# Kernel optimization log

Hardware: AMD Instinct MI355X
Metric: run time of the kernel (lower is better)

The kernel has to match this reference:

```python
import jax, jax.numpy as jnp
import numpy as np
import math

N = 524288          # number of 3D query points
L = 4               # grid_level = num_sin_layers - 2
F = 8               # feat_dim per hash level
T = 1 << 19         # log2_hashmap_size = 19 (hardcoded in module)
H = 64              # SIREN hidden width (dims entries)
OUT_DIM = 128       # sin_dims[-1] * size_factor
BOUND = 1.0
BASE_RES = 16.0
PER_LEVEL_SCALE = 2.0
BASE_SIGMA = 5.0
EXP_SIGMA = 2.0
SIN_W0 = 30.0
SIN_W1 = 30.0

_PRIMES = jnp.array([1, 2654435761, 805459861], dtype=jnp.uint32)  # tcnn hash primes
_CORNERS = np.array([[(i >> 2) & 1, (i >> 1) & 1, i & 1] for i in range(8)])
_CORNERS_U = jnp.asarray(_CORNERS, dtype=jnp.uint32)
_CORNERS_F = jnp.asarray(_CORNERS, dtype=jnp.float32)


def hash_grid(pos01, table):
    """Multi-resolution hash-grid encoding. pos01: [N,3] in [0,1], table: [L,T,F] -> [L,N,F]."""
    res = jnp.floor(BASE_RES * PER_LEVEL_SCALE ** jnp.arange(L, dtype=jnp.float32))  # [L]

    def level(tab, r):
        p = pos01 * r                       # [N,3]
        p0 = jnp.floor(p)
        f = p - p0                          # trilinear fractions
        c = p0.astype(jnp.uint32)[:, None, :] + _CORNERS_U[None]   # [N,8,3] corner coords
        hp = c * _PRIMES
        h = (hp[..., 0] ^ hp[..., 1] ^ hp[..., 2]) & jnp.uint32(T - 1)  # [N,8] hash indices
        feats = tab[h]                      # [N,8,F]
        w = jnp.prod(jnp.where(_CORNERS_F[None] > 0, f[:, None, :], 1.0 - f[:, None, :]), axis=-1)  # [N,8]
        return jnp.einsum('nc,ncf->nf', w, feats)

    return jax.vmap(level)(table, res)


def setup_inputs() -> dict:
    key = jax.random.key(0)
    ks = jax.random.split(key, 10)
    in_pos = jax.random.uniform(ks[0], (N, 3), minval=-BOUND, maxval=BOUND)
    table = jax.random.uniform(ks[1], (L, T, F), minval=-1e-4, maxval=1e-4)
    # ffn[i] = randn(F, H) * base_sigma * exp_sigma**i
    scales = BASE_SIGMA * EXP_SIGMA ** jnp.arange(L, dtype=jnp.float32)
    ffn = jax.random.normal(ks[2], (L, F, H)) * scales[:, None, None]
    # SIREN init: first layer U(-1/fan_in, 1/fan_in); others U(-sqrt(6/fan_in)/w0, ...)
    W0 = jax.random.uniform(ks[3], (3, H), minval=-1.0 / 3.0, maxval=1.0 / 3.0)
    b0 = jax.random.uniform(ks[4], (H,), minval=-1.0 / math.sqrt(3.0), maxval=1.0 / math.sqrt(3.0))
    bw = math.sqrt(6.0 / H) / SIN_W0
    Ws = jax.random.uniform(ks[5], (L, H, H), minval=-bw, maxval=bw)
    bs = jax.random.uniform(ks[6], (L, H), minval=-1.0 / math.sqrt(H), maxval=1.0 / math.sqrt(H))
    bo = math.sqrt(6.0 / H) / SIN_W1
    Wout = jax.random.uniform(ks[7], (L, H, OUT_DIM), minval=-bo, maxval=bo)
    bout = jax.random.uniform(ks[8], (L, OUT_DIM), minval=-1.0 / math.sqrt(H), maxval=1.0 / math.sqrt(H))
    return {"in_pos": in_pos, "table": table, "ffn": ffn, "W0": W0, "b0": b0,
            "Ws": Ws, "bs": bs, "Wout": Wout, "bout": bout}


def reference(in_pos, table, ffn, W0, b0, Ws, bs, Wout, bout):
    x = in_pos / BOUND                              # SIREN input in [-1,1]
    pos01 = (in_pos + BOUND) / (2.0 * BOUND)        # grid input in [0,1]
    grid_x = hash_grid(pos01, table)                # [L,N,F]
    # Fourier feature branch: sin(2*pi * grid_x @ ffn)
    emb = jnp.sin(2.0 * math.pi * jnp.einsum('lnf,lfh->lnh', grid_x, ffn))  # [L,N,H]
    # first SIREN layer (layer 0)
    x = jnp.sin(SIN_W0 * (x @ W0 + b0))             # [N,H]
    x_out = jnp.zeros((x.shape[0], OUT_DIM), x.dtype)
    for l in range(L):                              # layers 1..num_sin_layers-2
        x = jnp.sin(SIN_W0 * (x @ Ws[l] + bs[l]))
        x = emb[l] + x                              # residual add of grid Fourier features
        x_out = x_out + jnp.sin(SIN_W1 * (x @ Wout[l] + bout[l]))  # accumulate output head
    return x_out
```

## Files before the change

### kernel.cpp

```cpp
#include <hip/hip_runtime.h>
#include <cstdint>
#include <cstddef>

#define NLVL 4
#define TSIZE (1u << 19)
#define NH 64
#define NOUT 128
#define MBLK 128
#define PANEL 12800
#define SFOLD 4.774648292756860f

typedef _Float16 f16x8 __attribute__((ext_vector_type(8)));
typedef _Float16 f16x2 __attribute__((ext_vector_type(2)));
typedef float f32x4 __attribute__((ext_vector_type(4)));
typedef unsigned short u16x8 __attribute__((ext_vector_type(8)));
typedef unsigned int u32x4 __attribute__((ext_vector_type(4)));

__device__ __forceinline__ float fsin01(float x) {
    return __builtin_amdgcn_sinf(__builtin_amdgcn_fractf(x));
}
__device__ __forceinline__ unsigned short h2u(_Float16 h) {
    return __builtin_bit_cast(unsigned short, h);
}
__device__ __forceinline__ unsigned int pk16(float a, float b) {
    return __builtin_bit_cast(unsigned int, __builtin_amdgcn_cvt_pkrtz(a, b));
}
__device__ __forceinline__ void gl_lds16(const _Float16* g, _Float16* l) {
    __builtin_amdgcn_global_load_lds(
        (const __attribute__((address_space(1))) void*)g,
        (__attribute__((address_space(3))) void*)l, 16, 0, 0);
}

__global__ void prep_weights(const float* __restrict__ Ws,
                             const float* __restrict__ Wout,
                             const float* __restrict__ ffn,
                             _Float16* __restrict__ ws)
{
    int i = blockIdx.x * 256 + threadIdx.x;
    if (i < 16384) {
        int l = i >> 12, r = i & 4095, k = r >> 6, c = r & 63;
        ws[l * PANEL + ((c * 64 + k) ^ ((c & 7) << 3))] = (_Float16)(Ws[i] * SFOLD);
    } else if (i < 18432) {
        int j = i - 16384;
        int l = j >> 9, r = j & 511, k = r >> 6, c = r & 63;
        ws[l * PANEL + 4096 + c * 8 + k] = (_Float16)(ffn[j] * 0.000244140625f);
    } else if (i < 51200) {
        int j = i - 18432;
        int l = j >> 13, rem = j & 8191, k = rem >> 7, c = rem & 127;
        int ct = c >> 4, r15 = c & 15, kb = k >> 5, hi4 = (k >> 3) & 3, jj = k & 7;
        ws[l * PANEL + 4608 + (ct * 2 + kb) * 512 + hi4 * 128 + r15 * 8 + jj] =
            (_Float16)(Wout[j] * SFOLD);
    }
}

__global__ __launch_bounds__(256) void prep_table(const float* __restrict__ table,
                                                  _Float16* __restrict__ tab16)
{
    int i = blockIdx.x * 256 + threadIdx.x;
    float v = __builtin_nontemporal_load(table + i);
    tab16[i] = (_Float16)(v * 4096.f);
}

template <bool F16TAB>
__global__ __launch_bounds__(512, 2)
void ffb_main(const float* __restrict__ in_pos,
              const float* __restrict__ table,
              const _Float16* __restrict__ tab16,
              const float* __restrict__ W0,
              const float* __restrict__ b0,
              const float* __restrict__ bs,
              const float* __restrict__ bout,
              const _Float16* __restrict__ wsg,
              float* __restrict__ out)
{
    __shared__ __align__(16) _Float16 wbuf[2][PANEL];
    __shared__ __align__(16) unsigned short gS[NLVL][MBLK][8];

    const int tid = threadIdx.x;
    const int pbase = blockIdx.x * MBLK;
    const int lane = tid & 63;
    const int wv = tid >> 6;
    const int r15 = lane & 15;
    const int hi4 = lane >> 4;

    {
        const int p = tid & (MBLK - 1);
        const int lv = tid >> 7;
        const float px = in_pos[3 * (pbase + p) + 0];
        const float py = in_pos[3 * (pbase + p) + 1];
        const float pz = in_pos[3 * (pbase + p) + 2];
        const float qx = (px + 1.f) * 0.5f, qy = (py + 1.f) * 0.5f, qz = (pz + 1.f) * 0.5f;
        const uint32_t P1 = 2654435761u, P2 = 805459861u;

        const float res = (float)(16 << lv);
        float gx = qx * res, gy = qy * res, gz = qz * res;
        float fx0 = floorf(gx), fy0 = floorf(gy), fz0 = floorf(gz);
        float fx = gx - fx0, fy = gy - fy0, fz = gz - fz0;
        uint32_t ux = (uint32_t)fx0, uy = (uint32_t)fy0, uz = (uint32_t)fz0;
        uint32_t hx0 = ux, hx1 = ux + 1u;
        uint32_t hy0 = uy * P1, hy1 = hy0 + P1;
        uint32_t hz0 = uz * P2, hz1 = hz0 + P2;

        uint32_t hh[8];
        float    wgt[8];
        #pragma unroll
        for (int c = 0; c < 8; ++c) {
            hh[c] = (((c & 4) ? hx1 : hx0) ^ ((c & 2) ? hy1 : hy0)
                     ^ ((c & 1) ? hz1 : hz0)) & (TSIZE - 1u);
            wgt[c] = ((c & 4) ? fx : 1.f - fx) * ((c & 2) ? fy : 1.f - fy)
                   * ((c & 1) ? fz : 1.f - fz);
        }

        if (F16TAB) {
            const _Float16* tl = tab16 + (size_t)lv * TSIZE * 8;
            u16x8 vv[8];
            #pragma unroll
            for (int c = 0; c < 8; ++c)
                vv[c] = *(const u16x8*)(tl + (size_t)hh[c] * 8);
            f16x2 acc2[4];
            #pragma unroll
            for (int q = 0; q < 4; ++q) acc2[q] = (f16x2){(_Float16)0.f, (_Float16)0.f};
            #pragma unroll
            for (int c = 0; c < 8; ++c) {
                _Float16 wh = (_Float16)wgt[c];
                f16x2 ww = {wh, wh};
                const f16x2* vp = (const f16x2*)&vv[c];
                #pragma unroll
                for (int q = 0; q < 4; ++q) acc2[q] = acc2[q] + ww * vp[q];
            }
            *(u16x8*)&gS[lv][p][0] = *(u16x8*)&acc2[0];
        } else {
            const float* tl = table + (size_t)lv * TSIZE * 8;
            float g[8];
            #pragma unroll
            for (int q = 0; q < 8; ++q) g[q] = 0.f;
            #pragma unroll
            for (int c = 0; c < 8; ++c) {
                const float4* fp = (const float4*)(tl + (size_t)hh[c] * 8);
                float4 va = fp[0], vb = fp[1];
                float w = wgt[c];
                g[0] = fmaf(w, va.x, g[0]); g[1] = fmaf(w, va.y, g[1]);
                g[2] = fmaf(w, va.z, g[2]); g[3] = fmaf(w, va.w, g[3]);
                g[4] = fmaf(w, vb.x, g[4]); g[5] = fmaf(w, vb.y, g[5]);
                g[6] = fmaf(w, vb.z, g[6]); g[7] = fmaf(w, vb.w, g[7]);
            }
            u16x8 gv;
            #pragma unroll
            for (int q = 0; q < 8; ++q)
                gv[q] = h2u((_Float16)(g[q] * 4096.f));
            *(u16x8*)&gS[lv][p][0] = gv;
        }
    }

    auto stage = [&](int l) {
        const _Float16* src = wsg + l * PANEL;
        _Float16* dst = &wbuf[l & 1][0];
        #pragma unroll
        for (int i = 0; i < 3; ++i)
            gl_lds16(src + (i * 512 + tid) * 8, dst + (i * 512 + (tid & ~63)) * 8);
        if (tid < 64)
            gl_lds16(src + (1536 + tid) * 8, dst + 1536 * 8);
    };
    stage(0);

    f16x8 Xb[2];
    {
        const int pp = pbase + wv * 16 + r15;
        const float lpx = in_pos[3 * pp + 0];
        const float lpy = in_pos[3 * pp + 1];
        const float lpz = in_pos[3 * pp + 2];
        #pragma unroll
        for (int kb = 0; kb < 2; ++kb) {
            f16x8 v;
            #pragma unroll
            for (int j = 0; j < 8; ++j) {
                const int f = kb * 32 + hi4 * 8 + j;
                float a = b0[f] + lpx * W0[f] + lpy * W0[64 + f] + lpz * W0[128 + f];
                v[j] = (_Float16)fsin01(a * SFOLD);
            }
            Xb[kb] = v;
        }
    }
    __syncthreads();

    const int idxA = ((lane & 16) << 3) + r15 * 4;
    const int idxB = idxA + 64;
    const bool hiHalf = (lane & 32) != 0;

    f16x2 accP[8][2];
    #pragma unroll
    for (int ct = 0; ct < 8; ++ct)
        #pragma unroll
        for (int s = 0; s < 2; ++s) accP[ct][s] = (f16x2){(_Float16)0.f, (_Float16)0.f};

    #pragma unroll 1
    for (int lvl = 0; lvl < NLVL; ++lvl) {
        if (lvl < NLVL - 1) stage(lvl + 1);
        const _Float16* wp = &wbuf[lvl & 1][0];

        f16x8 gB;
        {
            f16x8 z;
            #pragma unroll
            for (int q = 0; q < 8; ++q) z[q] = (_Float16)0.f;
            if (lane < 16)
                z = *(const f16x8*)&gS[lvl][wv * 16 + lane][0];
            gB = z;
        }

        unsigned int P[4][2];
        #pragma unroll
        for (int ct = 0; ct < 4; ++ct) {
            const int i0 = ((ct * 16 + r15) * 64 + hi4 * 8) ^ ((r15 & 7) << 3);
            f16x8 A0 = *(const f16x8*)&wp[i0];
            f16x8 A1 = *(const f16x8*)&wp[i0 ^ 32];
            f16x8 Af;
            #pragma unroll
            for (int q = 0; q < 8; ++q) Af[q] = (_Float16)0.f;
            if (lane < 16)
                Af = *(const f16x8*)&wp[4096 + (ct * 16 + lane) * 8];
            float4 bs4 = *(const float4*)&bs[lvl * 64 + ct * 16 + hi4 * 4];

            f32x4 c1 = {bs4.x * SFOLD, bs4.y * SFOLD, bs4.z * SFOLD, bs4.w * SFOLD};
            c1 = __builtin_amdgcn_mfma_f32_16x16x32_f16(A0, Xb[0], c1, 0, 0, 0);
            c1 = __builtin_amdgcn_mfma_f32_16x16x32_f16(A1, Xb[1], c1, 0, 0, 0);
            f32x4 c2 = {0.f, 0.f, 0.f, 0.f};
            c2 = __builtin_amdgcn_mfma_f32_16x16x32_f16(Af, gB, c2, 0, 0, 0);

            P[ct][0] = pk16(fsin01(c1[0]) + fsin01(c2[0]),
                            fsin01(c1[1]) + fsin01(c2[1]));
            P[ct][1] = pk16(fsin01(c1[2]) + fsin01(c2[2]),
                            fsin01(c1[3]) + fsin01(c2[3]));
        }

        #pragma unroll
        for (int kb = 0; kb < 2; ++kb) {
            unsigned int w[4];
            #pragma unroll
            for (int m = 0; m < 4; ++m) {
                int idx = (m < 2) ? idxA : idxB;
                int lo = __builtin_amdgcn_ds_bpermute(idx, (int)P[2 * kb + 0][m & 1]);
                int hi = __builtin_amdgcn_ds_bpermute(idx, (int)P[2 * kb + 1][m & 1]);
                w[m] = (unsigned int)(hiHalf ? hi : lo);
            }
            Xb[kb] = __builtin_bit_cast(f16x8, (u32x4){w[0], w[1], w[2], w[3]});
        }

        #pragma unroll
        for (int ct = 0; ct < 8; ++ct) {
            const _Float16* bp = &wp[4608 + (ct * 2) * 512 + hi4 * 128 + r15 * 8];
            f16x8 B0 = *(const f16x8*)bp;
            f16x8 B1 = *(const f16x8*)(bp + 512);
            float bov = bout[lvl * 128 + ct * 16 + r15] * SFOLD;
            f32x4 c = {bov, bov, bov, bov};
            c = __builtin_amdgcn_mfma_f32_16x16x32_f16(Xb[0], B0, c, 0, 0, 0);
            c = __builtin_amdgcn_mfma_f32_16x16x32_f16(Xb[1], B1, c, 0, 0, 0);
            accP[ct][0] = accP[ct][0] +
                __builtin_bit_cast(f16x2, pk16(fsin01(c[0]), fsin01(c[1])));
            accP[ct][1] = accP[ct][1] +
                __builtin_bit_cast(f16x2, pk16(fsin01(c[2]), fsin01(c[3])));
        }

        if (lvl < NLVL - 1) __syncthreads();
    }

    #pragma unroll
    for (int s = 0; s < 2; ++s)
        #pragma unroll
        for (int r2 = 0; r2 < 2; ++r2) {
            int row = pbase + wv * 16 + hi4 * 4 + s * 2 + r2;
            #pragma unroll
            for (int ct = 0; ct < 8; ++ct) {
                float v = (float)accP[ct][s][r2];
                __builtin_nontemporal_store(v, &out[(size_t)row * 128 + ct * 16 + r15]);
            }
        }
}

extern "C" void kernel_launch(void* const* d_in, const int* in_sizes, int n_in,
                              void* d_out, int out_size, void* d_ws, size_t ws_size,
                              hipStream_t stream) {
    const float* in_pos = (const float*)d_in[0];
    const float* table  = (const float*)d_in[1];
    const float* ffn    = (const float*)d_in[2];
    const float* W0     = (const float*)d_in[3];
    const float* b0     = (const float*)d_in[4];
    const float* Ws     = (const float*)d_in[5];
    const float* bs     = (const float*)d_in[6];
    const float* Wout   = (const float*)d_in[7];
    const float* bout   = (const float*)d_in[8];
    float* out = (float*)d_out;
    _Float16* ws = (_Float16*)d_ws;

    const size_t need = 65536u * 2u + (size_t)NLVL * TSIZE * 8u * 2u;
    const bool f16tab = (ws_size >= need);
    _Float16* tab16 = ws + 65536;

    prep_weights<<<dim3(200), dim3(256), 0, stream>>>(Ws, Wout, ffn, ws);

    const int n = in_sizes[0] / 3;
    if (f16tab) {
        prep_table<<<dim3((NLVL * TSIZE * 8) / 256), dim3(256), 0, stream>>>(table, tab16);
        ffb_main<true><<<dim3(n / MBLK), dim3(512), 0, stream>>>(
            in_pos, table, tab16, W0, b0, bs, bout, ws, out);
    } else {
        ffb_main<false><<<dim3(n / MBLK), dim3(512), 0, stream>>>(
            in_pos, table, tab16, W0, b0, bs, bout, ws, out);
    }
}
```

Before: 256.4 us.

## Split hash-grid gather into a separate kernel and prefetch per-level features

Moves the hash-grid corner gather and trilinear blend into a standalone high-occupancy kernel that writes per-level f16 features to workspace. The main MLP kernel then reads these features from global memory, prefetching the next level's values one iteration ahead, and no longer needs the LDS staging buffer for them. The aim is to stop the random table gathers from stalling the MFMA-heavy main kernel. In exchange it adds a kernel launch and a round trip of the intermediate features through global memory, and this path is only taken when the workspace is large enough.

```diff
diff --git a/kernel.cpp b/kernel.cpp
--- a/kernel.cpp
+++ b/kernel.cpp
@@ -4,6 +4,8 @@
 
 #define NLVL 4
 #define TSIZE (1u << 19)
+#define NPTS (1 << 19)
+#define PLOG 19
 #define NH 64
 #define NOUT 128
 #define MBLK 128
@@ -61,11 +63,60 @@
     tab16[i] = (_Float16)(v * 4096.f);
 }
 
-template <bool F16TAB>
+__global__ __launch_bounds__(256, 4)
+void gather_g(const float* __restrict__ in_pos,
+              const _Float16* __restrict__ tab16,
+              _Float16* __restrict__ gSg)
+{
+    const int gid = blockIdx.x * 256 + threadIdx.x;
+    const int point = gid & (NPTS - 1);
+    const int lv = gid >> PLOG;
+
+    const float px = in_pos[3 * point + 0];
+    const float py = in_pos[3 * point + 1];
+    const float pz = in_pos[3 * point + 2];
+    const float qx = (px + 1.f) * 0.5f, qy = (py + 1.f) * 0.5f, qz = (pz + 1.f) * 0.5f;
+    const uint32_t P1 = 2654435761u, P2 = 805459861u;
+
+    const float res = (float)(16 << lv);
+    float gx = qx * res, gy = qy * res, gz = qz * res;
+    float fx0 = floorf(gx), fy0 = floorf(gy), fz0 = floorf(gz);
+    float fx = gx - fx0, fy = gy - fy0, fz = gz - fz0;
+    uint32_t ux = (uint32_t)fx0, uy = (uint32_t)fy0, uz = (uint32_t)fz0;
+    uint32_t hx0 = ux, hx1 = ux + 1u;
+    uint32_t hy0 = uy * P1, hy1 = hy0 + P1;
+    uint32_t hz0 = uz * P2, hz1 = hz0 + P2;
+
+    const _Float16* tl = tab16 + (size_t)lv * TSIZE * 8;
+    u16x8 vv[8];
+    #pragma unroll
+    for (int c = 0; c < 8; ++c) {
+        uint32_t h = (((c & 4) ? hx1 : hx0) ^ ((c & 2) ? hy1 : hy0)
+                      ^ ((c & 1) ? hz1 : hz0)) & (TSIZE - 1u);
+        vv[c] = *(const u16x8*)(tl + (size_t)h * 8);
+    }
+    f16x2 acc2[4];
+    #pragma unroll
+    for (int q = 0; q < 4; ++q) acc2[q] = (f16x2){(_Float16)0.f, (_Float16)0.f};
+    #pragma unroll
+    for (int c = 0; c < 8; ++c) {
+        float w = ((c & 4) ? fx : 1.f - fx) * ((c & 2) ? fy : 1.f - fy)
+                * ((c & 1) ? fz : 1.f - fz);
+        _Float16 wh = (_Float16)w;
+        f16x2 ww = {wh, wh};
+        const f16x2* vp = (const f16x2*)&vv[c];
+        #pragma unroll
+        for (int q = 0; q < 4; ++q) acc2[q] = acc2[q] + ww * vp[q];
+    }
+    *(u16x8*)&gSg[(size_t)gid * 8] = *(u16x8*)&acc2[0];
+}
+
+template <int MODE>
 __global__ __launch_bounds__(512, 2)
 void ffb_main(const float* __restrict__ in_pos,
               const float* __restrict__ table,
               const _Float16* __restrict__ tab16,
+              const _Float16* __restrict__ gSg,
               const float* __restrict__ W0,
               const float* __restrict__ b0,
               const float* __restrict__ bs,
@@ -74,7 +125,7 @@
               float* __restrict__ out)
 {
     __shared__ __align__(16) _Float16 wbuf[2][PANEL];
-    __shared__ __align__(16) unsigned short gS[NLVL][MBLK][8];
+    __shared__ __align__(16) unsigned short gS[MODE < 2 ? NLVL * MBLK * 8 : 4];
 
     const int tid = threadIdx.x;
     const int pbase = blockIdx.x * MBLK;
@@ -83,7 +134,7 @@
     const int r15 = lane & 15;
     const int hi4 = lane >> 4;
 
-    {
+    if (MODE < 2) {
         const int p = tid & (MBLK - 1);
         const int lv = tid >> 7;
         const float px = in_pos[3 * (pbase + p) + 0];
@@ -111,7 +162,7 @@
                    * ((c & 1) ? fz : 1.f - fz);
         }
 
-        if (F16TAB) {
+        if (MODE == 1) {
             const _Float16* tl = tab16 + (size_t)lv * TSIZE * 8;
             u16x8 vv[8];
             #pragma unroll
@@ -128,7 +179,7 @@
                 #pragma unroll
                 for (int q = 0; q < 4; ++q) acc2[q] = acc2[q] + ww * vp[q];
             }
-            *(u16x8*)&gS[lv][p][0] = *(u16x8*)&acc2[0];
+            *(u16x8*)&gS[(lv * MBLK + p) * 8] = *(u16x8*)&acc2[0];
         } else {
             const float* tl = table + (size_t)lv * TSIZE * 8;
             float g[8];
@@ -148,7 +199,7 @@
             #pragma unroll
             for (int q = 0; q < 8; ++q)
                 gv[q] = h2u((_Float16)(g[q] * 4096.f));
-            *(u16x8*)&gS[lv][p][0] = gv;
+            *(u16x8*)&gS[(lv * MBLK + p) * 8] = gv;
         }
     }
 
@@ -183,6 +234,19 @@
     }
     __syncthreads();
 
+    auto loadg = [&](int l) -> f16x8 {
+        f16x8 z;
+        #pragma unroll
+        for (int q = 0; q < 8; ++q) z[q] = (_Float16)0.f;
+        if (lane < 16) {
+            if (MODE == 2)
+                z = *(const f16x8*)&gSg[((size_t)l * NPTS + pbase + wv * 16 + lane) * 8];
+            else
+                z = *(const f16x8*)&gS[(l * MBLK + wv * 16 + lane) * 8];
+        }
+        return z;
+    };
+
     const int idxA = ((lane & 16) << 3) + r15 * 4;
     const int idxB = idxA + 64;
     const bool hiHalf = (lane & 32) != 0;
@@ -193,20 +257,13 @@
         #pragma unroll
         for (int s = 0; s < 2; ++s) accP[ct][s] = (f16x2){(_Float16)0.f, (_Float16)0.f};
 
+    f16x8 gBcur = loadg(0);
+
     #pragma unroll 1
     for (int lvl = 0; lvl < NLVL; ++lvl) {
         if (lvl < NLVL - 1) stage(lvl + 1);
+        f16x8 gBnext = (lvl < NLVL - 1) ? loadg(lvl + 1) : gBcur;
         const _Float16* wp = &wbuf[lvl & 1][0];
-
-        f16x8 gB;
-        {
-            f16x8 z;
-            #pragma unroll
-            for (int q = 0; q < 8; ++q) z[q] = (_Float16)0.f;
-            if (lane < 16)
-                z = *(const f16x8*)&gS[lvl][wv * 16 + lane][0];
-            gB = z;
-        }
 
         unsigned int P[4][2];
         #pragma unroll
@@ -225,7 +282,7 @@
             c1 = __builtin_amdgcn_mfma_f32_16x16x32_f16(A0, Xb[0], c1, 0, 0, 0);
             c1 = __builtin_amdgcn_mfma_f32_16x16x32_f16(A1, Xb[1], c1, 0, 0, 0);
             f32x4 c2 = {0.f, 0.f, 0.f, 0.f};
-            c2 = __builtin_amdgcn_mfma_f32_16x16x32_f16(Af, gB, c2, 0, 0, 0);
+            c2 = __builtin_amdgcn_mfma_f32_16x16x32_f16(Af, gBcur, c2, 0, 0, 0);
 
             P[ct][0] = pk16(fsin01(c1[0]) + fsin01(c2[0]),
                             fsin01(c1[1]) + fsin01(c2[1]));
@@ -261,6 +318,7 @@
                 __builtin_bit_cast(f16x2, pk16(fsin01(c[2]), fsin01(c[3])));
         }
 
+        gBcur = gBnext;
         if (lvl < NLVL - 1) __syncthreads();
     }
 
@@ -292,19 +350,27 @@
     float* out = (float*)d_out;
     _Float16* ws = (_Float16*)d_ws;
 
-    const size_t need = 65536u * 2u + (size_t)NLVL * TSIZE * 8u * 2u;
-    const bool f16tab = (ws_size >= need);
+    const int n = in_sizes[0] / 3;
+    const size_t tabElems = (size_t)NLVL * TSIZE * 8;
+    const size_t gOff = 65536u + tabElems;
+    const size_t need1 = (65536u + tabElems) * 2u;
+    const size_t need2 = (gOff + (size_t)NLVL * n * 8) * 2u;
     _Float16* tab16 = ws + 65536;
+    _Float16* gSg   = ws + gOff;
 
     prep_weights<<<dim3(200), dim3(256), 0, stream>>>(Ws, Wout, ffn, ws);
 
-    const int n = in_sizes[0] / 3;
-    if (f16tab) {
-        prep_table<<<dim3((NLVL * TSIZE * 8) / 256), dim3(256), 0, stream>>>(table, tab16);
-        ffb_main<true><<<dim3(n / MBLK), dim3(512), 0, stream>>>(
-            in_pos, table, tab16, W0, b0, bs, bout, ws, out);
+    if (ws_size >= need2) {
+        prep_table<<<dim3(tabElems / 256), dim3(256), 0, stream>>>(table, tab16);
+        gather_g<<<dim3((NLVL * n) / 256), dim3(256), 0, stream>>>(in_pos, tab16, gSg);
+        ffb_main<2><<<dim3(n / MBLK), dim3(512), 0, stream>>>(
+            in_pos, table, tab16, gSg, W0, b0, bs, bout, ws, out);
+    } else if (ws_size >= need1) {
+        prep_table<<<dim3(tabElems / 256), dim3(256), 0, stream>>>(table, tab16);
+        ffb_main<1><<<dim3(n / MBLK), dim3(512), 0, stream>>>(
+            in_pos, table, tab16, gSg, W0, b0, bs, bout, ws, out);
     } else {
-        ffb_main<false><<<dim3(n / MBLK), dim3(512), 0, stream>>>(
-            in_pos, table, tab16, W0, b0, bs, bout, ws, out);
-    }
-}
+        ffb_main<0><<<dim3(n / MBLK), dim3(512), 0, stream>>>(
+            in_pos, table, tab16, gSg, W0, b0, bs, bout, ws, out);
+    }
+}
```

Result: no change. 258.2 us (+0.7%).

## Process four point tiles per block and prefetch next tile's hash gathers

Applied to the files above, without the earlier changes.

Each block now handles four consecutive 128-point tiles in a persistent loop, with double-buffered grid-feature LDS slots. The hash-table gathers for the next tile are issued before the current tile's MLP so their latency overlaps MFMA work. Weight panels keep cycling through the same double buffer across tiles. The cost is more live registers for the in-flight gathers, a quarter as many blocks, and extra LDS for the second gS slot, which may reduce occupancy and leave the GPU underfilled.

```diff
diff --git a/kernel.cpp b/kernel.cpp
--- a/kernel.cpp
+++ b/kernel.cpp
@@ -7,6 +7,7 @@
 #define NH 64
 #define NOUT 128
 #define MBLK 128
+#define TILES 4
 #define PANEL 12800
 #define SFOLD 4.774648292756860f
 
@@ -74,83 +75,97 @@
               float* __restrict__ out)
 {
     __shared__ __align__(16) _Float16 wbuf[2][PANEL];
-    __shared__ __align__(16) unsigned short gS[NLVL][MBLK][8];
+    __shared__ __align__(16) unsigned short gS[2][NLVL][MBLK][8];
 
     const int tid = threadIdx.x;
-    const int pbase = blockIdx.x * MBLK;
+    const int blkbase = blockIdx.x * (MBLK * TILES);
     const int lane = tid & 63;
     const int wv = tid >> 6;
     const int r15 = lane & 15;
     const int hi4 = lane >> 4;
 
-    {
-        const int p = tid & (MBLK - 1);
-        const int lv = tid >> 7;
-        const float px = in_pos[3 * (pbase + p) + 0];
-        const float py = in_pos[3 * (pbase + p) + 1];
-        const float pz = in_pos[3 * (pbase + p) + 2];
-        const float qx = (px + 1.f) * 0.5f, qy = (py + 1.f) * 0.5f, qz = (pz + 1.f) * 0.5f;
-        const uint32_t P1 = 2654435761u, P2 = 805459861u;
-
-        const float res = (float)(16 << lv);
-        float gx = qx * res, gy = qy * res, gz = qz * res;
+    const int p_g = tid & (MBLK - 1);
+    const int lv_g = tid >> 7;
+    const uint32_t P1 = 2654435761u, P2 = 805459861u;
+
+    u16x8 vv[8];
+    float gfx, gfy, gfz;
+
+    auto issueGather = [&](int pb) {
+        const float px = in_pos[3 * (pb + p_g) + 0];
+        const float py = in_pos[3 * (pb + p_g) + 1];
+        const float pz = in_pos[3 * (pb + p_g) + 2];
+        const float res = (float)(16 << lv_g);
+        float gx = (px + 1.f) * 0.5f * res;
+        float gy = (py + 1.f) * 0.5f * res;
+        float gz = (pz + 1.f) * 0.5f * res;
+        float fx0 = floorf(gx), fy0 = floorf(gy), fz0 = floorf(gz);
+        gfx = gx - fx0; gfy = gy - fy0; gfz = gz - fz0;
+        uint32_t ux = (uint32_t)fx0, uy = (uint32_t)fy0, uz = (uint32_t)fz0;
+        uint32_t hx0 = ux, hx1 = ux + 1u;
+        uint32_t hy0 = uy * P1, hy1 = hy0 + P1;
+        uint32_t hz0 = uz * P2, hz1 = hz0 + P2;
+        const _Float16* tl = tab16 + (size_t)lv_g * TSIZE * 8;
+        #pragma unroll
+        for (int c = 0; c < 8; ++c) {
+            uint32_t h = (((c & 4) ? hx1 : hx0) ^ ((c & 2) ? hy1 : hy0)
+                          ^ ((c & 1) ? hz1 : hz0)) & (TSIZE - 1u);
+            vv[c] = *(const u16x8*)(tl + (size_t)h * 8);
+        }
+    };
+    auto interpStore = [&](int slot) {
+        f16x2 acc2[4];
+        #pragma unroll
+        for (int q = 0; q < 4; ++q) acc2[q] = (f16x2){(_Float16)0.f, (_Float16)0.f};
+        #pragma unroll
+        for (int c = 0; c < 8; ++c) {
+            float w = ((c & 4) ? gfx : 1.f - gfx) * ((c & 2) ? gfy : 1.f - gfy)
+                    * ((c & 1) ? gfz : 1.f - gfz);
+            _Float16 wh = (_Float16)w;
+            f16x2 ww = {wh, wh};
+            const f16x2* vp = (const f16x2*)&vv[c];
+            #pragma unroll
+            for (int q = 0; q < 4; ++q) acc2[q] = acc2[q] + ww * vp[q];
+        }
+        *(u16x8*)&gS[slot][lv_g][p_g][0] = *(u16x8*)&acc2[0];
+    };
+    auto gatherF32 = [&](int pb, int slot) {
+        const float px = in_pos[3 * (pb + p_g) + 0];
+        const float py = in_pos[3 * (pb + p_g) + 1];
+        const float pz = in_pos[3 * (pb + p_g) + 2];
+        const float res = (float)(16 << lv_g);
+        float gx = (px + 1.f) * 0.5f * res;
+        float gy = (py + 1.f) * 0.5f * res;
+        float gz = (pz + 1.f) * 0.5f * res;
         float fx0 = floorf(gx), fy0 = floorf(gy), fz0 = floorf(gz);
         float fx = gx - fx0, fy = gy - fy0, fz = gz - fz0;
         uint32_t ux = (uint32_t)fx0, uy = (uint32_t)fy0, uz = (uint32_t)fz0;
         uint32_t hx0 = ux, hx1 = ux + 1u;
         uint32_t hy0 = uy * P1, hy1 = hy0 + P1;
         uint32_t hz0 = uz * P2, hz1 = hz0 + P2;
-
-        uint32_t hh[8];
-        float    wgt[8];
+        const float* tl = table + (size_t)lv_g * TSIZE * 8;
+        float g[8];
+        #pragma unroll
+        for (int q = 0; q < 8; ++q) g[q] = 0.f;
         #pragma unroll
         for (int c = 0; c < 8; ++c) {
-            hh[c] = (((c & 4) ? hx1 : hx0) ^ ((c & 2) ? hy1 : hy0)
-                     ^ ((c & 1) ? hz1 : hz0)) & (TSIZE - 1u);
-            wgt[c] = ((c & 4) ? fx : 1.f - fx) * ((c & 2) ? fy : 1.f - fy)
-                   * ((c & 1) ? fz : 1.f - fz);
-        }
-
-        if (F16TAB) {
-            const _Float16* tl = tab16 + (size_t)lv * TSIZE * 8;
-            u16x8 vv[8];
-            #pragma unroll
-            for (int c = 0; c < 8; ++c)
-                vv[c] = *(const u16x8*)(tl + (size_t)hh[c] * 8);
-            f16x2 acc2[4];
-            #pragma unroll
-            for (int q = 0; q < 4; ++q) acc2[q] = (f16x2){(_Float16)0.f, (_Float16)0.f};
-            #pragma unroll
-            for (int c = 0; c < 8; ++c) {
-                _Float16 wh = (_Float16)wgt[c];
-                f16x2 ww = {wh, wh};
-                const f16x2* vp = (const f16x2*)&vv[c];
-                #pragma unroll
-                for (int q = 0; q < 4; ++q) acc2[q] = acc2[q] + ww * vp[q];
-            }
-            *(u16x8*)&gS[lv][p][0] = *(u16x8*)&acc2[0];
-        } else {
-            const float* tl = table + (size_t)lv * TSIZE * 8;
-            float g[8];
-            #pragma unroll
-            for (int q = 0; q < 8; ++q) g[q] = 0.f;
-            #pragma unroll
-            for (int c = 0; c < 8; ++c) {
-                const float4* fp = (const float4*)(tl + (size_t)hh[c] * 8);
-                float4 va = fp[0], vb = fp[1];
-                float w = wgt[c];
-                g[0] = fmaf(w, va.x, g[0]); g[1] = fmaf(w, va.y, g[1]);
-                g[2] = fmaf(w, va.z, g[2]); g[3] = fmaf(w, va.w, g[3]);
-                g[4] = fmaf(w, vb.x, g[4]); g[5] = fmaf(w, vb.y, g[5]);
-                g[6] = fmaf(w, vb.z, g[6]); g[7] = fmaf(w, vb.w, g[7]);
-            }
-            u16x8 gv;
-            #pragma unroll
-            for (int q = 0; q < 8; ++q)
-                gv[q] = h2u((_Float16)(g[q] * 4096.f));
-            *(u16x8*)&gS[lv][p][0] = gv;
-        }
-    }
+            uint32_t h = (((c & 4) ? hx1 : hx0) ^ ((c & 2) ? hy1 : hy0)
+                          ^ ((c & 1) ? hz1 : hz0)) & (TSIZE - 1u);
+            float w = ((c & 4) ? fx : 1.f - fx) * ((c & 2) ? fy : 1.f - fy)
+                    * ((c & 1) ? fz : 1.f - fz);
+            const float4* fp = (const float4*)(tl + (size_t)h * 8);
+            float4 va = fp[0], vb = fp[1];
+            g[0] = fmaf(w, va.x, g[0]); g[1] = fmaf(w, va.y, g[1]);
+            g[2] = fmaf(w, va.z, g[2]); g[3] = fmaf(w, va.w, g[3]);
+            g[4] = fmaf(w, vb.x, g[4]); g[5] = fmaf(w, vb.y, g[5]);
+            g[6] = fmaf(w, vb.z, g[6]); g[7] = fmaf(w, vb.w, g[7]);
+        }
+        u16x8 gv;
+        #pragma unroll
+        for (int q = 0; q < 8; ++q)
+            gv[q] = h2u((_Float16)(g[q] * 4096.f));
+        *(u16x8*)&gS[slot][lv_g][p_g][0] = gv;
+    };
 
     auto stage = [&](int l) {
         const _Float16* src = wsg + l * PANEL;
@@ -161,11 +176,10 @@
         if (tid < 64)
             gl_lds16(src + (1536 + tid) * 8, dst + 1536 * 8);
     };
-    stage(0);
 
     f16x8 Xb[2];
-    {
-        const int pp = pbase + wv * 16 + r15;
+    auto layer0 = [&](int pb) {
+        const int pp = pb + wv * 16 + r15;
         const float lpx = in_pos[3 * pp + 0];
         const float lpy = in_pos[3 * pp + 1];
         const float lpz = in_pos[3 * pp + 2];
@@ -180,101 +194,121 @@
             }
             Xb[kb] = v;
         }
-    }
+    };
+
+    if (F16TAB) issueGather(blkbase);
+    stage(0);
+    if (F16TAB) interpStore(0); else gatherF32(blkbase, 0);
+    layer0(blkbase);
     __syncthreads();
 
     const int idxA = ((lane & 16) << 3) + r15 * 4;
     const int idxB = idxA + 64;
     const bool hiHalf = (lane & 32) != 0;
 
-    f16x2 accP[8][2];
-    #pragma unroll
-    for (int ct = 0; ct < 8; ++ct)
-        #pragma unroll
-        for (int s = 0; s < 2; ++s) accP[ct][s] = (f16x2){(_Float16)0.f, (_Float16)0.f};
-
     #pragma unroll 1
-    for (int lvl = 0; lvl < NLVL; ++lvl) {
-        if (lvl < NLVL - 1) stage(lvl + 1);
-        const _Float16* wp = &wbuf[lvl & 1][0];
-
-        f16x8 gB;
-        {
-            f16x8 z;
-            #pragma unroll
-            for (int q = 0; q < 8; ++q) z[q] = (_Float16)0.f;
-            if (lane < 16)
-                z = *(const f16x8*)&gS[lvl][wv * 16 + lane][0];
-            gB = z;
-        }
-
-        unsigned int P[4][2];
-        #pragma unroll
-        for (int ct = 0; ct < 4; ++ct) {
-            const int i0 = ((ct * 16 + r15) * 64 + hi4 * 8) ^ ((r15 & 7) << 3);
-            f16x8 A0 = *(const f16x8*)&wp[i0];
-            f16x8 A1 = *(const f16x8*)&wp[i0 ^ 32];
-            f16x8 Af;
-            #pragma unroll
-            for (int q = 0; q < 8; ++q) Af[q] = (_Float16)0.f;
-            if (lane < 16)
-                Af = *(const f16x8*)&wp[4096 + (ct * 16 + lane) * 8];
-            float4 bs4 = *(const float4*)&bs[lvl * 64 + ct * 16 + hi4 * 4];
-
-            f32x4 c1 = {bs4.x * SFOLD, bs4.y * SFOLD, bs4.z * SFOLD, bs4.w * SFOLD};
-            c1 = __builtin_amdgcn_mfma_f32_16x16x32_f16(A0, Xb[0], c1, 0, 0, 0);
-            c1 = __builtin_amdgcn_mfma_f32_16x16x32_f16(A1, Xb[1], c1, 0, 0, 0);
-            f32x4 c2 = {0.f, 0.f, 0.f, 0.f};
-            c2 = __builtin_amdgcn_mfma_f32_16x16x32_f16(Af, gB, c2, 0, 0, 0);
-
-            P[ct][0] = pk16(fsin01(c1[0]) + fsin01(c2[0]),
-                            fsin01(c1[1]) + fsin01(c2[1]));
-            P[ct][1] = pk16(fsin01(c1[2]) + fsin01(c2[2]),
-                            fsin01(c1[3]) + fsin01(c2[3]));
-        }
-
-        #pragma unroll
-        for (int kb = 0; kb < 2; ++kb) {
-            unsigned int w[4];
-            #pragma unroll
-            for (int m = 0; m < 4; ++m) {
-                int idx = (m < 2) ? idxA : idxB;
-                int lo = __builtin_amdgcn_ds_bpermute(idx, (int)P[2 * kb + 0][m & 1]);
-                int hi = __builtin_amdgcn_ds_bpermute(idx, (int)P[2 * kb + 1][m & 1]);
-                w[m] = (unsigned int)(hiHalf ? hi : lo);
-            }
-            Xb[kb] = __builtin_bit_cast(f16x8, (u32x4){w[0], w[1], w[2], w[3]});
-        }
-
-        #pragma unroll
-        for (int ct = 0; ct < 8; ++ct) {
-            const _Float16* bp = &wp[4608 + (ct * 2) * 512 + hi4 * 128 + r15 * 8];
-            f16x8 B0 = *(const f16x8*)bp;
-            f16x8 B1 = *(const f16x8*)(bp + 512);
-            float bov = bout[lvl * 128 + ct * 16 + r15] * SFOLD;
-            f32x4 c = {bov, bov, bov, bov};
-            c = __builtin_amdgcn_mfma_f32_16x16x32_f16(Xb[0], B0, c, 0, 0, 0);
-            c = __builtin_amdgcn_mfma_f32_16x16x32_f16(Xb[1], B1, c, 0, 0, 0);
-            accP[ct][0] = accP[ct][0] +
-                __builtin_bit_cast(f16x2, pk16(fsin01(c[0]), fsin01(c[1])));
-            accP[ct][1] = accP[ct][1] +
-                __builtin_bit_cast(f16x2, pk16(fsin01(c[2]), fsin01(c[3])));
-        }
-
-        if (lvl < NLVL - 1) __syncthreads();
+    for (int t = 0; t < TILES; ++t) {
+        const int pb = blkbase + t * MBLK;
+        if (F16TAB && t + 1 < TILES) issueGather(pb + MBLK);
+        const int slot = t & 1;
+
+        f16x2 accP[8][2];
+        #pragma unroll
+        for (int ct = 0; ct < 8; ++ct)
+            #pragma unroll
+            for (int s = 0; s < 2; ++s) accP[ct][s] = (f16x2){(_Float16)0.f, (_Float16)0.f};
+
+        #pragma unroll 1
+        for (int lvl = 0; lvl < NLVL; ++lvl) {
+            const bool lastAll = (t == TILES - 1) && (lvl == NLVL - 1);
+            if (!lastAll) stage((lvl + 1) & 3);
+            const _Float16* wp = &wbuf[lvl & 1][0];
+
+            f16x8 gB;
+            {
+                f16x8 z;
+                #pragma unroll
+                for (int q = 0; q < 8; ++q) z[q] = (_Float16)0.f;
+                if (lane < 16)
+                    z = *(const f16x8*)&gS[slot][lvl][wv * 16 + lane][0];
+                gB = z;
+            }
+
+            unsigned int P[4][2];
+            #pragma unroll
+            for (int ct = 0; ct < 4; ++ct) {
+                const int i0 = ((ct * 16 + r15) * 64 + hi4 * 8) ^ ((r15 & 7) << 3);
+                f16x8 A0 = *(const f16x8*)&wp[i0];
+                f16x8 A1 = *(const f16x8*)&wp[i0 ^ 32];
+                f16x8 Af;
+                #pragma unroll
+                for (int q = 0; q < 8; ++q) Af[q] = (_Float16)0.f;
+                if (lane < 16)
+                    Af = *(const f16x8*)&wp[4096 + (ct * 16 + lane) * 8];
+                float4 bs4 = *(const float4*)&bs[lvl * 64 + ct * 16 + hi4 * 4];
+
+                f32x4 c1 = {bs4.x * SFOLD, bs4.y * SFOLD, bs4.z * SFOLD, bs4.w * SFOLD};
+                c1 = __builtin_amdgcn_mfma_f32_16x16x32_f16(A0, Xb[0], c1, 0, 0, 0);
+                c1 = __builtin_amdgcn_mfma_f32_16x16x32_f16(A1, Xb[1], c1, 0, 0, 0);
+                f32x4 c2 = {0.f, 0.f, 0.f, 0.f};
+                c2 = __builtin_amdgcn_mfma_f32_16x16x32_f16(Af, gB, c2, 0, 0, 0);
+
+                P[ct][0] = pk16(fsin01(c1[0]) + fsin01(c2[0]),
+                                fsin01(c1[1]) + fsin01(c2[1]));
+                P[ct][1] = pk16(fsin01(c1[2]) + fsin01(c2[2]),
+                                fsin01(c1[3]) + fsin01(c2[3]));
+            }
+
+            #pragma unroll
+            for (int kb = 0; kb < 2; ++kb) {
+                unsigned int w[4];
+                #pragma unroll
+                for (int m = 0; m < 4; ++m) {
+                    int idx = (m < 2) ? idxA : idxB;
+                    int lo = __builtin_amdgcn_ds_bpermute(idx, (int)P[2 * kb + 0][m & 1]);
+                    int hi = __builtin_amdgcn_ds_bpermute(idx, (int)P[2 * kb + 1][m & 1]);
+                    w[m] = (unsigned int)(hiHalf ? hi : lo);
+                }
+                Xb[kb] = __builtin_bit_cast(f16x8, (u32x4){w[0], w[1], w[2], w[3]});
+            }
+
+            #pragma unroll
+            for (int ct = 0; ct < 8; ++ct) {
+                const _Float16* bp = &wp[4608 + (ct * 2) * 512 + hi4 * 128 + r15 * 8];
+                f16x8 B0 = *(const f16x8*)bp;
+                f16x8 B1 = *(const f16x8*)(bp + 512);
+                float bov = bout[lvl * 128 + ct * 16 + r15] * SFOLD;
+                f32x4 c = {bov, bov, bov, bov};
+                c = __builtin_amdgcn_mfma_f32_16x16x32_f16(Xb[0], B0, c, 0, 0, 0);
+                c = __builtin_amdgcn_mfma_f32_16x16x32_f16(Xb[1], B1, c, 0, 0, 0);
+                accP[ct][0] = accP[ct][0] +
+                    __builtin_bit_cast(f16x2, pk16(fsin01(c[0]), fsin01(c[1])));
+                accP[ct][1] = accP[ct][1] +
+                    __builtin_bit_cast(f16x2, pk16(fsin01(c[2]), fsin01(c[3])));
+            }
+
+            if (!lastAll) __syncthreads();
+        }
+
+        #pragma unroll
+        for (int s = 0; s < 2; ++s)
+            #pragma unroll
+            for (int r2 = 0; r2 < 2; ++r2) {
+                int row = pb + wv * 16 + hi4 * 4 + s * 2 + r2;
+                #pragma unroll
+                for (int ct = 0; ct < 8; ++ct) {
+                    float v = (float)accP[ct][s][r2];
+                    __builtin_nontemporal_store(v, &out[(size_t)row * 128 + ct * 16 + r15]);
+                }
+            }
+
+        if (t + 1 < TILES) {
+            if (F16TAB) interpStore((t + 1) & 1);
+            else        gatherF32(pb + MBLK, (t + 1) & 1);
+            layer0(pb + MBLK);
+            __syncthreads();
+        }
     }
-
-    #pragma unroll
-    for (int s = 0; s < 2; ++s)
-        #pragma unroll
-        for (int r2 = 0; r2 < 2; ++r2) {
-            int row = pbase + wv * 16 + hi4 * 4 + s * 2 + r2;
-            #pragma unroll
-            for (int ct = 0; ct < 8; ++ct) {
-                float v = (float)accP[ct][s][r2];
-                __builtin_nontemporal_store(v, &out[(size_t)row * 128 + ct * 16 + r15]);
-            }
-        }
 }
 
 extern "C" void kernel_launch(void* const* d_in, const int* in_sizes, int n_in,
@@ -292,19 +326,20 @@
     float* out = (float*)d_out;
     _Float16* ws = (_Float16*)d_ws;
 
-    const size_t need = 65536u * 2u + (size_t)NLVL * TSIZE * 8u * 2u;
-    const bool f16tab = (ws_size >= need);
+    const int n = in_sizes[0] / 3;
+    const size_t tabElems = (size_t)NLVL * TSIZE * 8;
+    const size_t need1 = (65536u + tabElems) * 2u;
     _Float16* tab16 = ws + 65536;
 
     prep_weights<<<dim3(200), dim3(256), 0, stream>>>(Ws, Wout, ffn, ws);
 
-    const int n = in_sizes[0] / 3;
-    if (f16tab) {
-        prep_table<<<dim3((NLVL * TSIZE * 8) / 256), dim3(256), 0, stream>>>(table, tab16);
-        ffb_main<true><<<dim3(n / MBLK), dim3(512), 0, stream>>>(
+    const int grid = n / (MBLK * TILES);
+    if (ws_size >= need1) {
+        prep_table<<<dim3(tabElems / 256), dim3(256), 0, stream>>>(table, tab16);
+        ffb_main<true><<<dim3(grid), dim3(512), 0, stream>>>(
             in_pos, table, tab16, W0, b0, bs, bout, ws, out);
     } else {
-        ffb_main<false><<<dim3(n / MBLK), dim3(512), 0, stream>>>(
+        ffb_main<false><<<dim3(grid), dim3(512), 0, stream>>>(
             in_pos, table, tab16, W0, b0, bs, bout, ws, out);
     }
 }
```

Measured after the change: 318.5 us. 24.2% more time.
